# Kernel optimization log

Hardware: AMD Instinct MI355X
Metric: run time of the kernel (lower is better)

## Reference

```python
import jax, jax.numpy as jnp
from jax import lax
import numpy as np

T, I, H, O = 2048, 2048, 4096, 1


def setup_inputs() -> dict:
    key = jax.random.key(0)
    ks = jax.random.split(key, 7)
    s_ih = 1.0 / np.sqrt(I)
    s_hh = 1.0 / np.sqrt(H)
    return {
        "inputSequence": jax.random.normal(ks[0], (T, I), jnp.float32),
        "W_ih": jax.random.normal(ks[1], (4 * H, I), jnp.float32) * s_ih,
        "W_hh": jax.random.normal(ks[2], (4 * H, H), jnp.float32) * s_hh,
        "b_ih": jax.random.normal(ks[3], (4 * H,), jnp.float32) * s_hh,
        "b_hh": jax.random.normal(ks[4], (4 * H,), jnp.float32) * s_hh,
        "W_lin": jax.random.normal(ks[5], (O, H), jnp.float32) * s_hh,
        "b_lin": jax.random.normal(ks[6], (O,), jnp.float32) * s_hh,
    }


def reference(inputSequence, W_ih, W_hh, b_ih, b_hh, W_lin, b_lin):
    # torch.nn.LSTMCell semantics, unbatched; dropout p=0 -> identity.
    hidden = W_hh.shape[1]

    def step(carry, x):
        h, c = carry
        gates = W_ih @ x + b_ih + W_hh @ h + b_hh  # [4H]
        i, f, g, o = jnp.split(gates, 4)
        i = jax.nn.sigmoid(i)
        f = jax.nn.sigmoid(f)
        g = jnp.tanh(g)
        o = jax.nn.sigmoid(o)
        c = f * c + i * g
        h = o * jnp.tanh(c)
        p = jax.nn.sigmoid(W_lin @ h + b_lin)[0]  # pAction[t] = output[0]
        return (h, c), p

    init = (jnp.zeros((hidden,), inputSequence.dtype),
            jnp.zeros((hidden,), inputSequence.dtype))
    _, pAction = lax.scan(step, init, inputSequence)
    return pAction  # [T]; action/reward lists are empty when isSimulation=False
```

## Files before the change

kernel.cpp:

```cpp
#include <hip/hip_runtime.h>

typedef short  short8 __attribute__((ext_vector_type(8)));
typedef float  f32x4  __attribute__((ext_vector_type(4)));
typedef _Float16 half8_t __attribute__((ext_vector_type(8)));
typedef _Float16 half2_t __attribute__((ext_vector_type(2)));

#define T_STEPS 2048
#define I_DIM   2048
#define H_DIM   4096
#define G_DIM   16384

__device__ __forceinline__ unsigned short f2bf(float x) {
    union { float f; unsigned int u; } v; v.f = x;
    unsigned int u = v.u;
    return (unsigned short)((u + 0x7FFFu + ((u >> 16) & 1u)) >> 16);
}
__device__ __forceinline__ float sigmoidf_(float x) {
    return 1.0f / (1.0f + __expf(-x));
}

__device__ __forceinline__ float dot2f(half2_t a, half2_t b, float acc) {
#if __has_builtin(__builtin_amdgcn_fdot2)
    return __builtin_amdgcn_fdot2(a, b, acc, false);
#else
    return fmaf((float)a[0], (float)b[0], fmaf((float)a[1], (float)b[1], acc));
#endif
}
__device__ __forceinline__ float dot8f(half8_t a, half8_t b, float acc) {
    acc = dot2f(__builtin_shufflevector(a, a, 0, 1), __builtin_shufflevector(b, b, 0, 1), acc);
    acc = dot2f(__builtin_shufflevector(a, a, 2, 3), __builtin_shufflevector(b, b, 2, 3), acc);
    acc = dot2f(__builtin_shufflevector(a, a, 4, 5), __builtin_shufflevector(b, b, 4, 5), acc);
    acc = dot2f(__builtin_shufflevector(a, a, 6, 7), __builtin_shufflevector(b, b, 6, 7), acc);
    return acc;
}

__global__ void convert_f32_f16(const float* __restrict__ in,
                                _Float16* __restrict__ out, int n8) {
    int i = blockIdx.x * blockDim.x + threadIdx.x;
    int stride = gridDim.x * blockDim.x;
    for (; i < n8; i += stride) {
        f32x4 a = *(const f32x4*)(in + (size_t)i * 8);
        f32x4 b = *(const f32x4*)(in + (size_t)i * 8 + 4);
        half8_t o;
        o[0] = (_Float16)a[0]; o[1] = (_Float16)a[1];
        o[2] = (_Float16)a[2]; o[3] = (_Float16)a[3];
        o[4] = (_Float16)b[0]; o[5] = (_Float16)b[1];
        o[6] = (_Float16)b[2]; o[7] = (_Float16)b[3];
        *(half8_t*)(out + (size_t)i * 8) = o;
    }
}

__global__ void zero_f32(float* __restrict__ p, int n) {
    int i = blockIdx.x * blockDim.x + threadIdx.x;
    int stride = gridDim.x * blockDim.x;
    for (; i < n; i += stride) p[i] = 0.0f;
}

__device__ __forceinline__ short8 cvt8(const float* __restrict__ p) {
    f32x4 a = *(const f32x4*)p;
    f32x4 b = *(const f32x4*)(p + 4);
    short8 r;
    r[0] = (short)f2bf(a[0]); r[1] = (short)f2bf(a[1]);
    r[2] = (short)f2bf(a[2]); r[3] = (short)f2bf(a[3]);
    r[4] = (short)f2bf(b[0]); r[5] = (short)f2bf(b[1]);
    r[6] = (short)f2bf(b[2]); r[7] = (short)f2bf(b[3]);
    return r;
}

__global__ __launch_bounds__(256) void gemm_bt(const float* __restrict__ A,
                                               const float* __restrict__ B,
                                               const float* __restrict__ bih,
                                               const float* __restrict__ bhh,
                                               _Float16* __restrict__ C,
                                               int M, int N, int K) {
    __shared__ unsigned short As[128 * 32];
    __shared__ unsigned short Bs[128 * 32];
    const int bn = blockIdx.x, bm = blockIdx.y;
    const int tid = threadIdx.x;
    const int w = tid >> 6, l = tid & 63;
    const int wm = (w >> 1) * 64, wn = (w & 1) * 64;
    const int lr = l & 15, lk = (l >> 4) * 8;

    f32x4 acc[4][4];
#pragma unroll
    for (int mi = 0; mi < 4; mi++)
#pragma unroll
        for (int ni = 0; ni < 4; ni++) acc[mi][ni] = (f32x4)0.0f;

    const float* Ablk = A + (size_t)bm * 128 * K;
    const float* Bblk = B + (size_t)bn * 128 * K;

    for (int k0 = 0; k0 < K; k0 += 32) {
#pragma unroll
        for (int s = 0; s < 2; ++s) {
            int ch = tid + s * 256;
            int r = ch >> 2, kc = (ch & 3) * 8;
            ((short8*)As)[ch] = cvt8(Ablk + (size_t)r * K + k0 + kc);
            ((short8*)Bs)[ch] = cvt8(Bblk + (size_t)r * K + k0 + kc);
        }
        __syncthreads();
        short8 af[4], bfr[4];
#pragma unroll
        for (int mi = 0; mi < 4; mi++)
            af[mi] = *(const short8*)&As[(wm + mi * 16 + lr) * 32 + lk];
#pragma unroll
        for (int ni = 0; ni < 4; ni++)
            bfr[ni] = *(const short8*)&Bs[(wn + ni * 16 + lr) * 32 + lk];
#pragma unroll
        for (int mi = 0; mi < 4; mi++)
#pragma unroll
            for (int ni = 0; ni < 4; ni++)
                acc[mi][ni] = __builtin_amdgcn_mfma_f32_16x16x32_bf16(
                    af[mi], bfr[ni], acc[mi][ni], 0, 0, 0);
        __syncthreads();
    }

    const int cr = (l >> 4) * 4, cc = l & 15;
#pragma unroll
    for (int mi = 0; mi < 4; mi++) {
#pragma unroll
        for (int ni = 0; ni < 4; ni++) {
            int col = bn * 128 + wn + ni * 16 + cc;
            float bias = bih[col] + bhh[col];
#pragma unroll
            for (int r = 0; r < 4; r++) {
                int row = bm * 128 + wm + mi * 16 + cr + r;
                C[(size_t)row * N + col] = (_Float16)(acc[mi][ni][r] + bias);
            }
        }
    }
}

__global__ __launch_bounds__(512, 2) void lstm_seq(
        const _Float16* __restrict__ W,
        const _Float16* __restrict__ G,
        const float* __restrict__ Wlin,
        _Float16* __restrict__ hbuf,
        unsigned* __restrict__ flags,
        float* __restrict__ praw_part) {
    extern __shared__ char smem[];
    _Float16* wl  = (_Float16*)smem;
    _Float16* hl  = (_Float16*)(smem + 131072);
    float*    part = (float*)(smem + 131072 + 8192);
    unsigned* hl32 = (unsigned*)hl;

    const int tid = threadIdx.x;
    const int w = tid >> 6, l = tid & 63;
    const int bid = blockIdx.x;
    const int base = bid * 16;

    half8_t wr[8][6];
#pragma unroll
    for (int rr = 0; rr < 8; ++rr) {
        const int rl = w * 8 + rr;
        const size_t grow = (size_t)((rl >> 4) * H_DIM + base + (rl & 15));
        const _Float16* wp = W + grow * H_DIM + l * 8;
#pragma unroll
        for (int c = 0; c < 6; ++c) {
            f32x4 tmp;
            asm volatile("global_load_dwordx4 %0, %1, off"
                         : "=v"(tmp) : "v"(wp + c * 512));
            wr[rr][c] = __builtin_bit_cast(half8_t, tmp);
        }
    }
    asm volatile("s_waitcnt vmcnt(0)" ::: "memory");
    __builtin_amdgcn_sched_barrier(0);

    for (int i = tid; i < 8192; i += 512) {
        int col8 = i & 63;
        int cr   = i >> 6;
        int rl = cr >> 1, c2 = cr & 1;
        size_t grow = (size_t)((rl >> 4) * H_DIM + base + (rl & 15));
        *(half8_t*)(wl + cr * 512 + col8 * 8) =
            *(const half8_t*)(W + grow * H_DIM + (6 + c2) * 512 + col8 * 8);
    }

    const float wlin = (tid < 16) ? Wlin[base + tid] : 0.0f;
    const int grow_g = (tid >> 4) * H_DIM + base + (tid & 15);
    const _Float16* wlbase = wl + (w * 16) * 512 + l * 8;
    const _Float16* hlbase = hl + l * 8;
    unsigned short* hb16 = (unsigned short*)hbuf;

    float creg = 0.0f;

#pragma unroll 1
    for (int t = 0; t < T_STEPS; ++t) {
        float gval = 0.0f;
        if (tid < 64) gval = (float)G[(size_t)t * G_DIM + grow_g];

        const unsigned* hsrc = (const unsigned*)hbuf + ((t & 1) << 11);
#pragma unroll
        for (int k = 0; k < 4; ++k)
            hl32[k * 512 + tid] = __hip_atomic_load(hsrc + k * 512 + tid,
                                                    __ATOMIC_RELAXED,
                                                    __HIP_MEMORY_SCOPE_AGENT);
        __syncthreads();

        float acc[8];
#pragma unroll
        for (int rr = 0; rr < 8; ++rr) acc[rr] = 0.0f;

#pragma unroll
        for (int c = 0; c < 6; ++c) {
            half8_t hv = *(const half8_t*)(hlbase + c * 512);
#pragma unroll
            for (int rr = 0; rr < 8; ++rr)
                acc[rr] = dot8f(wr[rr][c], hv, acc[rr]);
        }
#pragma unroll
        for (int c2 = 0; c2 < 2; ++c2) {
            half8_t hv = *(const half8_t*)(hlbase + (6 + c2) * 512);
#pragma unroll
            for (int rr = 0; rr < 8; ++rr) {
                half8_t wv = *(const half8_t*)(wlbase + (rr * 2 + c2) * 512);
                acc[rr] = dot8f(wv, hv, acc[rr]);
            }
        }
#pragma unroll
        for (int rr = 0; rr < 8; ++rr)
            part[(w * 8 + rr) * 65 + l] = acc[rr];
        __syncthreads();

        if (tid < 64) {
            const float* pr = part + tid * 65;
            float s0 = 0.f, s1 = 0.f, s2 = 0.f, s3 = 0.f;
#pragma unroll
            for (int j = 0; j < 16; ++j) {
                s0 += pr[4 * j + 0]; s1 += pr[4 * j + 1];
                s2 += pr[4 * j + 2]; s3 += pr[4 * j + 3];
            }
            float s = (s0 + s1) + (s2 + s3) + gval;
            float fv = __shfl(s, (tid & 15) + 16);
            float gv = __shfl(s, (tid & 15) + 32);
            float ov = __shfl(s, (tid & 15) + 48);
            if (tid < 16) {
                float c = sigmoidf_(fv) * creg + sigmoidf_(s) * tanhf(gv);
                creg = c;
                float hv = sigmoidf_(ov) * tanhf(c);
                unsigned short hb = __builtin_bit_cast(unsigned short, (_Float16)hv);
                __hip_atomic_store(hb16 + (((t + 1) & 1) << 12) + base + tid, hb,
                                   __ATOMIC_RELAXED, __HIP_MEMORY_SCOPE_AGENT);
                float pp = hv * wlin;
                pp += __shfl_xor(pp, 8, 16);
                pp += __shfl_xor(pp, 4, 16);
                pp += __shfl_xor(pp, 2, 16);
                pp += __shfl_xor(pp, 1, 16);
                if (tid == 0) praw_part[(size_t)bid * T_STEPS + t] = pp;
            }
        }

        if (w == 0) {
            asm volatile("s_waitcnt vmcnt(0)" ::: "memory");
            if (tid == 0)
                __hip_atomic_store(flags + bid, (unsigned)(t + 1),
                                   __ATOMIC_RELAXED, __HIP_MEMORY_SCOPE_AGENT);
            const unsigned tgt = (unsigned)(t + 1);
            for (;;) {
                unsigned f0 = __hip_atomic_load(flags + l,       __ATOMIC_RELAXED, __HIP_MEMORY_SCOPE_AGENT);
                unsigned f1 = __hip_atomic_load(flags + l + 64,  __ATOMIC_RELAXED, __HIP_MEMORY_SCOPE_AGENT);
                unsigned f2 = __hip_atomic_load(flags + l + 128, __ATOMIC_RELAXED, __HIP_MEMORY_SCOPE_AGENT);
                unsigned f3 = __hip_atomic_load(flags + l + 192, __ATOMIC_RELAXED, __HIP_MEMORY_SCOPE_AGENT);
                bool ok = (f0 >= tgt) & (f1 >= tgt) & (f2 >= tgt) & (f3 >= tgt);
                if (__all(ok)) break;
                __builtin_amdgcn_s_sleep(1);
            }
        }
        __syncthreads();
    }
}

__global__ void finalize_out(const float* __restrict__ praw_part,
                             const float* __restrict__ blin,
                             float* __restrict__ out, int n) {
    int i = blockIdx.x * blockDim.x + threadIdx.x;
    if (i < n) {
        float s = blin[0];
        for (int wg = 0; wg < 256; ++wg)
            s += praw_part[(size_t)wg * T_STEPS + i];
        out[i] = 1.0f / (1.0f + __expf(-s));
    }
}

extern "C" void kernel_launch(void* const* d_in, const int* in_sizes, int n_in,
                              void* d_out, int out_size, void* d_ws, size_t ws_size,
                              hipStream_t stream) {
    const float* X    = (const float*)d_in[0];
    const float* Wih  = (const float*)d_in[1];
    const float* Whh  = (const float*)d_in[2];
    const float* bih  = (const float*)d_in[3];
    const float* bhh  = (const float*)d_in[4];
    const float* Wlin = (const float*)d_in[5];
    const float* blin = (const float*)d_in[6];
    float* out = (float*)d_out;

    char* ws = (char*)d_ws;
    _Float16* Whh16 = (_Float16*)(ws);
    _Float16* G     = (_Float16*)(ws + 134217728);
    unsigned* flags = (unsigned*)(ws + 201326592);
    _Float16* hbuf  = (_Float16*)(ws + 201327616);
    float* praw_part = (float*)(ws + 201344000);

    convert_f32_f16<<<dim3(2048), dim3(256), 0, stream>>>(Whh, Whh16,
                                                          (16384 * 4096) / 8);
    zero_f32<<<dim3(17), dim3(256), 0, stream>>>((float*)flags, 4352);
    gemm_bt<<<dim3(128, 16), dim3(256), 0, stream>>>(X, Wih, bih, bhh, G,
                                                     2048, 16384, 2048);

    hipFuncSetAttribute((const void*)lstm_seq,
                        hipFuncAttributeMaxDynamicSharedMemorySize, 160 * 1024);

    void* args[] = { (void*)&Whh16, (void*)&G, (void*)&Wlin,
                     (void*)&hbuf, (void*)&flags, (void*)&praw_part };
    hipLaunchCooperativeKernel((void*)lstm_seq, dim3(256), dim3(512),
                               args, 155904, stream);

    finalize_out<<<dim3(8), dim3(256), 0, stream>>>(praw_part, blin, out, 2048);
}
```

Baseline: 17.69 ms.

## Store recurrent weights as scaled FP8 E4M3 and pad sync flags

Quantizes W_hh to FP8 E4M3 with a fixed scale of 256 instead of FP16. This halves the weight footprint, so the register- and LDS-resident weight split becomes half registers and half LDS rather than 6:2 chunks. The inner dot product now decodes FP8 pairs to f32 and uses scalar FMAs in place of packed fp16 dot2 instructions. Per-block sync flags are padded to a 32-word stride to reduce contention on shared cache lines. The trade-off is more ALU work per step (conversions plus twice the FMA count) and lower weight precision over a 2048-step recurrence.

```diff
diff --git a/kernel.cpp b/kernel.cpp
--- a/kernel.cpp
+++ b/kernel.cpp
@@ -2,13 +2,17 @@
 
 typedef short  short8 __attribute__((ext_vector_type(8)));
 typedef float  f32x4  __attribute__((ext_vector_type(4)));
+typedef float  f32x2  __attribute__((ext_vector_type(2)));
 typedef _Float16 half8_t __attribute__((ext_vector_type(8)));
-typedef _Float16 half2_t __attribute__((ext_vector_type(2)));
+typedef unsigned int u32x2 __attribute__((ext_vector_type(2)));
 
 #define T_STEPS 2048
 #define I_DIM   2048
 #define H_DIM   4096
 #define G_DIM   16384
+#define W_SCALE     256.0f
+#define W_INV_SCALE (1.0f / 256.0f)
+#define FLAG_STRIDE 32
 
 __device__ __forceinline__ unsigned short f2bf(float x) {
     union { float f; unsigned int u; } v; v.f = x;
@@ -19,34 +23,51 @@
     return 1.0f / (1.0f + __expf(-x));
 }
 
-__device__ __forceinline__ float dot2f(half2_t a, half2_t b, float acc) {
-#if __has_builtin(__builtin_amdgcn_fdot2)
-    return __builtin_amdgcn_fdot2(a, b, acc, false);
+__device__ __forceinline__ float dec1_e4m3(unsigned b) {
+    int e = (b >> 3) & 15, m = b & 7;
+    float v = (e == 0) ? ldexpf((float)m, -9) : ldexpf((float)(8 + m), e - 10);
+    return (b & 0x80) ? -v : v;
+}
+template <bool HI>
+__device__ __forceinline__ f32x2 fp8pair_f32(unsigned w) {
+#if __has_builtin(__builtin_amdgcn_cvt_pk_f32_fp8)
+    return __builtin_amdgcn_cvt_pk_f32_fp8((int)w, HI);
 #else
-    return fmaf((float)a[0], (float)b[0], fmaf((float)a[1], (float)b[1], acc));
+    unsigned sh = HI ? 16u : 0u;
+    f32x2 r;
+    r[0] = dec1_e4m3((w >> sh) & 0xFF);
+    r[1] = dec1_e4m3((w >> (sh + 8)) & 0xFF);
+    return r;
 #endif
 }
-__device__ __forceinline__ float dot8f(half8_t a, half8_t b, float acc) {
-    acc = dot2f(__builtin_shufflevector(a, a, 0, 1), __builtin_shufflevector(b, b, 0, 1), acc);
-    acc = dot2f(__builtin_shufflevector(a, a, 2, 3), __builtin_shufflevector(b, b, 2, 3), acc);
-    acc = dot2f(__builtin_shufflevector(a, a, 4, 5), __builtin_shufflevector(b, b, 4, 5), acc);
-    acc = dot2f(__builtin_shufflevector(a, a, 6, 7), __builtin_shufflevector(b, b, 6, 7), acc);
-    return acc;
-}
-
-__global__ void convert_f32_f16(const float* __restrict__ in,
-                                _Float16* __restrict__ out, int n8) {
+
+__device__ unsigned enc_e4m3(float x) {
+    float a = fabsf(x);
+    unsigned s = (__builtin_bit_cast(unsigned, x) >> 31) << 7;
+    if (a >= 448.0f) return s | 0x7E;
+    if (a < 0.015625f) {
+        int m = (int)rintf(a * 512.0f);
+        return s | (unsigned)(m > 7 ? 8 : m);
+    }
+    int e; float fr = frexpf(a, &e);
+    int q = (int)rintf(fr * 16.0f);
+    if (q == 16) { q = 8; e++; }
+    int e8 = e - 1 + 7;
+    if (e8 > 15 || (e8 == 15 && (q - 8) > 6)) return s | 0x7E;
+    return s | (unsigned)(e8 << 3) | (unsigned)(q - 8);
+}
+
+__global__ void convert_f32_fp8(const float* __restrict__ in,
+                                unsigned* __restrict__ out, int n4) {
     int i = blockIdx.x * blockDim.x + threadIdx.x;
     int stride = gridDim.x * blockDim.x;
-    for (; i < n8; i += stride) {
-        f32x4 a = *(const f32x4*)(in + (size_t)i * 8);
-        f32x4 b = *(const f32x4*)(in + (size_t)i * 8 + 4);
-        half8_t o;
-        o[0] = (_Float16)a[0]; o[1] = (_Float16)a[1];
-        o[2] = (_Float16)a[2]; o[3] = (_Float16)a[3];
-        o[4] = (_Float16)b[0]; o[5] = (_Float16)b[1];
-        o[6] = (_Float16)b[2]; o[7] = (_Float16)b[3];
-        *(half8_t*)(out + (size_t)i * 8) = o;
+    for (; i < n4; i += stride) {
+        f32x4 v = *(const f32x4*)(in + (size_t)i * 4);
+        unsigned b0 = enc_e4m3(v[0] * W_SCALE);
+        unsigned b1 = enc_e4m3(v[1] * W_SCALE);
+        unsigned b2 = enc_e4m3(v[2] * W_SCALE);
+        unsigned b3 = enc_e4m3(v[3] * W_SCALE);
+        out[i] = b0 | (b1 << 8) | (b2 << 16) | (b3 << 24);
     }
 }
 
@@ -132,14 +153,14 @@
 }
 
 __global__ __launch_bounds__(512, 2) void lstm_seq(
-        const _Float16* __restrict__ W,
+        const unsigned char* __restrict__ W8,
         const _Float16* __restrict__ G,
         const float* __restrict__ Wlin,
         _Float16* __restrict__ hbuf,
         unsigned* __restrict__ flags,
         float* __restrict__ praw_part) {
     extern __shared__ char smem[];
-    _Float16* wl  = (_Float16*)smem;
+    unsigned char* wl8 = (unsigned char*)smem;
     _Float16* hl  = (_Float16*)(smem + 131072);
     float*    part = (float*)(smem + 131072 + 8192);
     unsigned* hl32 = (unsigned*)hl;
@@ -149,35 +170,33 @@
     const int bid = blockIdx.x;
     const int base = bid * 16;
 
-    half8_t wr[8][6];
+    u32x2 wq[8][4];
 #pragma unroll
     for (int rr = 0; rr < 8; ++rr) {
         const int rl = w * 8 + rr;
         const size_t grow = (size_t)((rl >> 4) * H_DIM + base + (rl & 15));
-        const _Float16* wp = W + grow * H_DIM + l * 8;
-#pragma unroll
-        for (int c = 0; c < 6; ++c) {
-            f32x4 tmp;
-            asm volatile("global_load_dwordx4 %0, %1, off"
+        const unsigned char* wp = W8 + grow * 4096 + l * 8;
+#pragma unroll
+        for (int c = 0; c < 4; ++c) {
+            u32x2 tmp;
+            asm volatile("global_load_dwordx2 %0, %1, off"
                          : "=v"(tmp) : "v"(wp + c * 512));
-            wr[rr][c] = __builtin_bit_cast(half8_t, tmp);
+            wq[rr][c] = tmp;
         }
     }
     asm volatile("s_waitcnt vmcnt(0)" ::: "memory");
     __builtin_amdgcn_sched_barrier(0);
 
-    for (int i = tid; i < 8192; i += 512) {
-        int col8 = i & 63;
-        int cr   = i >> 6;
-        int rl = cr >> 1, c2 = cr & 1;
-        size_t grow = (size_t)((rl >> 4) * H_DIM + base + (rl & 15));
-        *(half8_t*)(wl + cr * 512 + col8 * 8) =
-            *(const half8_t*)(W + grow * H_DIM + (6 + c2) * 512 + col8 * 8);
+    for (int i = tid; i < 32768; i += 512) {
+        int r = i >> 9, cd = i & 511;
+        size_t grow = (size_t)((r >> 4) * H_DIM + base + (r & 15));
+        ((unsigned*)wl8)[r * 512 + cd] =
+            *(const unsigned*)(W8 + grow * 4096 + 2048 + cd * 4);
     }
 
     const float wlin = (tid < 16) ? Wlin[base + tid] : 0.0f;
     const int grow_g = (tid >> 4) * H_DIM + base + (tid & 15);
-    const _Float16* wlbase = wl + (w * 16) * 512 + l * 8;
+    const unsigned char* wlbase = wl8 + (size_t)(w * 8) * 2048 + l * 8;
     const _Float16* hlbase = hl + l * 8;
     unsigned short* hb16 = (unsigned short*)hbuf;
 
@@ -201,19 +220,46 @@
         for (int rr = 0; rr < 8; ++rr) acc[rr] = 0.0f;
 
 #pragma unroll
-        for (int c = 0; c < 6; ++c) {
+        for (int c = 0; c < 4; ++c) {
             half8_t hv = *(const half8_t*)(hlbase + c * 512);
-#pragma unroll
-            for (int rr = 0; rr < 8; ++rr)
-                acc[rr] = dot8f(wr[rr][c], hv, acc[rr]);
-        }
-#pragma unroll
-        for (int c2 = 0; c2 < 2; ++c2) {
-            half8_t hv = *(const half8_t*)(hlbase + (6 + c2) * 512);
+            float h0 = (float)hv[0], h1 = (float)hv[1], h2 = (float)hv[2], h3 = (float)hv[3];
+            float h4 = (float)hv[4], h5 = (float)hv[5], h6 = (float)hv[6], h7 = (float)hv[7];
 #pragma unroll
             for (int rr = 0; rr < 8; ++rr) {
-                half8_t wv = *(const half8_t*)(wlbase + (rr * 2 + c2) * 512);
-                acc[rr] = dot8f(wv, hv, acc[rr]);
+                f32x2 w01 = fp8pair_f32<false>(wq[rr][c][0]);
+                f32x2 w23 = fp8pair_f32<true >(wq[rr][c][0]);
+                f32x2 w45 = fp8pair_f32<false>(wq[rr][c][1]);
+                f32x2 w67 = fp8pair_f32<true >(wq[rr][c][1]);
+                acc[rr] = fmaf(w01[0], h0, acc[rr]);
+                acc[rr] = fmaf(w01[1], h1, acc[rr]);
+                acc[rr] = fmaf(w23[0], h2, acc[rr]);
+                acc[rr] = fmaf(w23[1], h3, acc[rr]);
+                acc[rr] = fmaf(w45[0], h4, acc[rr]);
+                acc[rr] = fmaf(w45[1], h5, acc[rr]);
+                acc[rr] = fmaf(w67[0], h6, acc[rr]);
+                acc[rr] = fmaf(w67[1], h7, acc[rr]);
+            }
+        }
+#pragma unroll
+        for (int c = 0; c < 4; ++c) {
+            half8_t hv = *(const half8_t*)(hlbase + (4 + c) * 512);
+            float h0 = (float)hv[0], h1 = (float)hv[1], h2 = (float)hv[2], h3 = (float)hv[3];
+            float h4 = (float)hv[4], h5 = (float)hv[5], h6 = (float)hv[6], h7 = (float)hv[7];
+#pragma unroll
+            for (int rr = 0; rr < 8; ++rr) {
+                u32x2 wv = *(const u32x2*)(wlbase + rr * 2048 + c * 512);
+                f32x2 w01 = fp8pair_f32<false>(wv[0]);
+                f32x2 w23 = fp8pair_f32<true >(wv[0]);
+                f32x2 w45 = fp8pair_f32<false>(wv[1]);
+                f32x2 w67 = fp8pair_f32<true >(wv[1]);
+                acc[rr] = fmaf(w01[0], h0, acc[rr]);
+                acc[rr] = fmaf(w01[1], h1, acc[rr]);
+                acc[rr] = fmaf(w23[0], h2, acc[rr]);
+                acc[rr] = fmaf(w23[1], h3, acc[rr]);
+                acc[rr] = fmaf(w45[0], h4, acc[rr]);
+                acc[rr] = fmaf(w45[1], h5, acc[rr]);
+                acc[rr] = fmaf(w67[0], h6, acc[rr]);
+                acc[rr] = fmaf(w67[1], h7, acc[rr]);
             }
         }
 #pragma unroll
@@ -229,7 +275,7 @@
                 s0 += pr[4 * j + 0]; s1 += pr[4 * j + 1];
                 s2 += pr[4 * j + 2]; s3 += pr[4 * j + 3];
             }
-            float s = (s0 + s1) + (s2 + s3) + gval;
+            float s = ((s0 + s1) + (s2 + s3)) * W_INV_SCALE + gval;
             float fv = __shfl(s, (tid & 15) + 16);
             float gv = __shfl(s, (tid & 15) + 32);
             float ov = __shfl(s, (tid & 15) + 48);
@@ -252,14 +298,14 @@
         if (w == 0) {
             asm volatile("s_waitcnt vmcnt(0)" ::: "memory");
             if (tid == 0)
-                __hip_atomic_store(flags + bid, (unsigned)(t + 1),
+                __hip_atomic_store(flags + (size_t)bid * FLAG_STRIDE, (unsigned)(t + 1),
                                    __ATOMIC_RELAXED, __HIP_MEMORY_SCOPE_AGENT);
             const unsigned tgt = (unsigned)(t + 1);
             for (;;) {
-                unsigned f0 = __hip_atomic_load(flags + l,       __ATOMIC_RELAXED, __HIP_MEMORY_SCOPE_AGENT);
-                unsigned f1 = __hip_atomic_load(flags + l + 64,  __ATOMIC_RELAXED, __HIP_MEMORY_SCOPE_AGENT);
-                unsigned f2 = __hip_atomic_load(flags + l + 128, __ATOMIC_RELAXED, __HIP_MEMORY_SCOPE_AGENT);
-                unsigned f3 = __hip_atomic_load(flags + l + 192, __ATOMIC_RELAXED, __HIP_MEMORY_SCOPE_AGENT);
+                unsigned f0 = __hip_atomic_load(flags + (size_t)l * FLAG_STRIDE,         __ATOMIC_RELAXED, __HIP_MEMORY_SCOPE_AGENT);
+                unsigned f1 = __hip_atomic_load(flags + (size_t)(l + 64) * FLAG_STRIDE,  __ATOMIC_RELAXED, __HIP_MEMORY_SCOPE_AGENT);
+                unsigned f2 = __hip_atomic_load(flags + (size_t)(l + 128) * FLAG_STRIDE, __ATOMIC_RELAXED, __HIP_MEMORY_SCOPE_AGENT);
+                unsigned f3 = __hip_atomic_load(flags + (size_t)(l + 192) * FLAG_STRIDE, __ATOMIC_RELAXED, __HIP_MEMORY_SCOPE_AGENT);
                 bool ok = (f0 >= tgt) & (f1 >= tgt) & (f2 >= tgt) & (f3 >= tgt);
                 if (__all(ok)) break;
                 __builtin_amdgcn_s_sleep(1);
@@ -294,22 +340,22 @@
     float* out = (float*)d_out;
 
     char* ws = (char*)d_ws;
-    _Float16* Whh16 = (_Float16*)(ws);
-    _Float16* G     = (_Float16*)(ws + 134217728);
-    unsigned* flags = (unsigned*)(ws + 201326592);
-    _Float16* hbuf  = (_Float16*)(ws + 201327616);
-    float* praw_part = (float*)(ws + 201344000);
-
-    convert_f32_f16<<<dim3(2048), dim3(256), 0, stream>>>(Whh, Whh16,
-                                                          (16384 * 4096) / 8);
-    zero_f32<<<dim3(17), dim3(256), 0, stream>>>((float*)flags, 4352);
+    unsigned char* W8 = (unsigned char*)(ws);
+    _Float16* G     = (_Float16*)(ws + 67108864);
+    unsigned* flags = (unsigned*)(ws + 134217728);
+    _Float16* hbuf  = (_Float16*)(ws + 134250496);
+    float* praw_part = (float*)(ws + 134266880);
+
+    convert_f32_fp8<<<dim3(2048), dim3(256), 0, stream>>>(Whh, (unsigned*)W8,
+                                                          (16384 * 4096) / 4);
+    zero_f32<<<dim3(48), dim3(256), 0, stream>>>((float*)flags, 12288);
     gemm_bt<<<dim3(128, 16), dim3(256), 0, stream>>>(X, Wih, bih, bhh, G,
                                                      2048, 16384, 2048);
 
     hipFuncSetAttribute((const void*)lstm_seq,
                         hipFuncAttributeMaxDynamicSharedMemorySize, 160 * 1024);
 
-    void* args[] = { (void*)&Whh16, (void*)&G, (void*)&Wlin,
+    void* args[] = { (void*)&W8, (void*)&G, (void*)&Wlin,
                      (void*)&hbuf, (void*)&flags, (void*)&praw_part };
     hipLaunchCooperativeKernel((void*)lstm_seq, dim3(256), dim3(512),
                                args, 155904, stream);
```

Result: slower. 29.89 ms (+69.0%).
